# Kernel tuning notes

Hardware: AMD Instinct MI355X
Metric: run time of the kernel (lower is better)

Reference implementation:

```python
import jax, jax.numpy as jnp
import numpy as np

P = 16          # patch_size
C = 3           # in_chans
D = 768         # embed_dim
V = 10240       # position_embedding_size
B, H, W = 16, 512, 512
N = (H // P) * (W // P)  # 1024 patches per image


def setup_inputs() -> dict:
    key = jax.random.key(0)
    k1, k2, k3, k4, k5 = jax.random.split(key, 5)
    pixel_values = jax.random.uniform(k1, (B, C, H, W), dtype=jnp.float32)
    position_ids = jax.random.randint(k2, (B, N, 2), 0, 32)  # (x, y) patch coords < pW/pH
    padding_positions = jax.random.randint(k3, (B, N), 0, 2).astype(jnp.bool_)
    w_proj = jax.random.normal(k4, (D, C * P * P), dtype=jnp.float32) * 0.02  # Linear weight (out, in)
    pos_table = jax.random.normal(k5, (2, V, D), dtype=jnp.float32) * 0.02
    return {
        "pixel_values": pixel_values,
        "w_proj": w_proj,
        "pos_table": pos_table,
        "position_ids": position_ids,
        "padding_positions": padding_positions,
    }


def reference(pixel_values, w_proj, pos_table, position_ids, padding_positions):
    b, c, h, w = pixel_values.shape
    ph, pw = h // P, w // P
    # Extract patches in Gemma4 C-P-P flatten order: (B, N, C*P*P)
    x = pixel_values.reshape(b, c, ph, P, pw, P)
    x = jnp.transpose(x, (0, 2, 4, 1, 3, 5)).reshape(b, ph * pw, c * P * P)
    patches = 2.0 * (x - 0.5)
    hidden = jnp.einsum('bnf,df->bnd', patches, w_proj)
    # Position embeddings: one_hot(ids) @ table summed over the 2 axes
    # == direct gather-add: table[0][x_id] + table[1][y_id]
    ids = jnp.clip(position_ids, 0)
    pos = pos_table[0][ids[..., 0]] + pos_table[1][ids[..., 1]]  # (B, N, D)
    pos = jnp.where(padding_positions[..., None], 0.0, pos)
    return hidden + pos
```

## Files before the change

kernel.cpp:

```cpp
#include <hip/hip_runtime.h>
#include <stdint.h>


typedef __attribute__((ext_vector_type(8))) short bfrag_t;
typedef __attribute__((ext_vector_type(4))) float f4_t;
typedef __attribute__((ext_vector_type(8))) unsigned short u16x8;

#define M_TOT 16384
#define K_TOT 768
#define N_TOT 768
#define V_POS 10240

__device__ __forceinline__ unsigned short f2bf(float f) {
    unsigned int u = __float_as_uint(f);
    u += 0x7fffu + ((u >> 16) & 1u);
    return (unsigned short)(u >> 16);
}

__device__ __forceinline__ void async_ld16(const void* g, void* l) {
    __builtin_amdgcn_global_load_lds(
        (const __attribute__((address_space(1))) void*)g,
        (__attribute__((address_space(3))) void*)l,
        16, 0, 0);
}

__global__ __launch_bounds__(256) void prep_kernel(
    const float* __restrict__ px, const float* __restrict__ wp,
    const void* __restrict__ pad_in,
    unsigned short* __restrict__ A, unsigned short* __restrict__ Wb,
    unsigned char* __restrict__ mask)
{
    int bid = blockIdx.x;
    int tid = threadIdx.x;
    if (bid < 6144) {
        long idx = (long)bid * 256 + tid;
        const float4* s = (const float4*)(px + (idx << 3));
        float4 v0 = s[0];
        float4 v1 = s[1];
        int w8 = (int)(idx & 63);
        int h  = (int)((idx >> 6) & 511);
        int bc = (int)(idx >> 15);
        int c = bc % 3, b = bc / 3;
        int m = b * 1024 + (h >> 4) * 32 + (w8 >> 1);
        int k = c * 256 + (h & 15) * 16 + ((w8 & 1) << 3);
        u16x8 o;
        o[0] = f2bf(2.f * v0.x - 1.f);
        o[1] = f2bf(2.f * v0.y - 1.f);
        o[2] = f2bf(2.f * v0.z - 1.f);
        o[3] = f2bf(2.f * v0.w - 1.f);
        o[4] = f2bf(2.f * v1.x - 1.f);
        o[5] = f2bf(2.f * v1.y - 1.f);
        o[6] = f2bf(2.f * v1.z - 1.f);
        o[7] = f2bf(2.f * v1.w - 1.f);
        *(u16x8*)(A + (long)m * K_TOT + k) = o;
    } else if (bid < 6432) {
        long idx = (long)(bid - 6144) * 256 + tid;
        const float4* s = (const float4*)(wp + (idx << 3));
        float4 v0 = s[0];
        float4 v1 = s[1];
        u16x8 o;
        o[0] = f2bf(v0.x); o[1] = f2bf(v0.y); o[2] = f2bf(v0.z); o[3] = f2bf(v0.w);
        o[4] = f2bf(v1.x); o[5] = f2bf(v1.y); o[6] = f2bf(v1.z); o[7] = f2bf(v1.w);
        *(u16x8*)(Wb + (idx << 3)) = o;
    } else {
        __shared__ int u8mode;
        if (tid == 0) u8mode = 0;
        __syncthreads();
        const unsigned int* pi = (const unsigned int*)pad_in;
        int local = 0;
        for (int i = tid; i < 4096; i += 256)
            if (pi[i] > 1u) local = 1;
        if (local) atomicOr(&u8mode, 1);
        __syncthreads();
        if (u8mode) {
            const unsigned char* p8 = (const unsigned char*)pad_in;
            for (int i = tid; i < M_TOT; i += 256) mask[i] = p8[i];
        } else {
            const int* p32 = (const int*)pad_in;
            for (int i = tid; i < M_TOT; i += 256) mask[i] = (unsigned char)(p32[i] != 0);
        }
    }
}

__global__ __launch_bounds__(256) void gemm_kernel(
    const unsigned short* __restrict__ A, const unsigned short* __restrict__ Bt,
    const int* __restrict__ pos_ids, const unsigned char* __restrict__ mask,
    const float* __restrict__ pos_table, float* __restrict__ out)
{
    __shared__ unsigned short As[128 * 32];
    __shared__ unsigned short Bs[128 * 32];

    int tid  = threadIdx.x;
    int wave = tid >> 6;
    int lane = tid & 63;
    int bm = blockIdx.x / 6, bn = blockIdx.x % 6;
    int m0 = bm * 128, n0 = bn * 128;

    int srow = lane >> 2;
    int scol = (lane & 3) << 3;
    int ch0  = wave * 2;
    const unsigned short* ga0 = A  + (size_t)(m0 + ch0 * 16 +      srow) * K_TOT + scol;
    const unsigned short* ga1 = A  + (size_t)(m0 + ch0 * 16 + 16 + srow) * K_TOT + scol;
    const unsigned short* gb0 = Bt + (size_t)(n0 + ch0 * 16 +      srow) * K_TOT + scol;
    const unsigned short* gb1 = Bt + (size_t)(n0 + ch0 * 16 + 16 + srow) * K_TOT + scol;
    unsigned short* la0 = &As[ch0 * 512];
    unsigned short* la1 = &As[ch0 * 512 + 512];
    unsigned short* lb0 = &Bs[ch0 * 512];
    unsigned short* lb1 = &Bs[ch0 * 512 + 512];

    int row_off = (wave & 1) << 6;
    int col_off = (wave >> 1) << 6;
    int fr = lane & 15;
    int qk = (lane >> 4) << 3;

    f4_t acc[4][4] = {};

    for (int kk = 0; kk < K_TOT / 32; ++kk) {
        int k0 = kk * 32;
        async_ld16(ga0 + k0, la0);
        async_ld16(ga1 + k0, la1);
        async_ld16(gb0 + k0, lb0);
        async_ld16(gb1 + k0, lb1);
        __syncthreads();

        bfrag_t a[4], b[4];
#pragma unroll
        for (int i = 0; i < 4; ++i)
            a[i] = *(const bfrag_t*)&As[(row_off + i * 16 + fr) * 32 + qk];
#pragma unroll
        for (int i = 0; i < 4; ++i)
            b[i] = *(const bfrag_t*)&Bs[(col_off + i * 16 + fr) * 32 + qk];
#pragma unroll
        for (int mi = 0; mi < 4; ++mi)
#pragma unroll
            for (int ni = 0; ni < 4; ++ni)
                acc[mi][ni] = __builtin_amdgcn_mfma_f32_16x16x32_bf16(
                    a[mi], b[ni], acc[mi][ni], 0, 0, 0);
        __syncthreads();
    }

    int quad = lane >> 4;
#pragma unroll
    for (int mi = 0; mi < 4; ++mi) {
#pragma unroll
        for (int reg = 0; reg < 4; ++reg) {
            int r = m0 + row_off + mi * 16 + quad * 4 + reg;
            int xid = pos_ids[2 * r];
            int yid = pos_ids[2 * r + 1];
            xid = xid < 0 ? 0 : xid;
            yid = yid < 0 ? 0 : yid;
            bool p = mask[r] != 0;
            const float* t0 = pos_table + (size_t)xid * N_TOT;
            const float* t1 = pos_table + (size_t)(V_POS + yid) * N_TOT;
            float* orow = out + (size_t)r * N_TOT;
#pragma unroll
            for (int ni = 0; ni < 4; ++ni) {
                int cidx = n0 + col_off + ni * 16 + fr;
                float pos = p ? 0.f : (t0[cidx] + t1[cidx]);
                orow[cidx] = acc[mi][ni][reg] + pos;
            }
        }
    }
}

extern "C" void kernel_launch(void* const* d_in, const int* in_sizes, int n_in,
                              void* d_out, int out_size, void* d_ws, size_t ws_size,
                              hipStream_t stream) {
    const float* px  = (const float*)d_in[0];
    const float* wp  = (const float*)d_in[1];
    const float* pt  = (const float*)d_in[2];
    const int*   pid = (const int*)d_in[3];
    const void*  pad = d_in[4];

    unsigned short* A    = (unsigned short*)d_ws;
    unsigned short* Wb   = A + (size_t)M_TOT * K_TOT;
    unsigned char*  mask = (unsigned char*)(Wb + (size_t)N_TOT * K_TOT);

    prep_kernel<<<6433, 256, 0, stream>>>(px, wp, pad, A, Wb, mask);
    gemm_kernel<<<(M_TOT / 128) * (N_TOT / 128), 256, 0, stream>>>(
        A, Wb, pid, mask, pt, (float*)d_out);
}
```

Measured before the change: 194.1 us.

## Fuse patch extraction into GEMM, stage full-K A tile in LDS, stream B from global

Pixel patch extraction and bf16 conversion now happen inside the GEMM kernel: each block loads one row of 32 patches into LDS with a padded stride, so the bf16 A matrix is no longer written to and re-read from global memory. B fragments are read straight from global/L2 into registers with software double-buffering, and each block loops over all 768 output columns. This removes a large intermediate round trip and one heavy prep pass. The cost is only 512 blocks with a small 32-row M tile, which gives low MFMA reuse per B load and may leave the GPU underoccupied.

```diff
diff --git a/kernel.cpp b/kernel.cpp
--- a/kernel.cpp
+++ b/kernel.cpp
@@ -5,11 +5,13 @@
 typedef __attribute__((ext_vector_type(8))) short bfrag_t;
 typedef __attribute__((ext_vector_type(4))) float f4_t;
 typedef __attribute__((ext_vector_type(8))) unsigned short u16x8;
+typedef __attribute__((ext_vector_type(4))) unsigned short u16x4;
 
 #define M_TOT 16384
 #define K_TOT 768
 #define N_TOT 768
 #define V_POS 10240
+#define A_STRIDE 776
 
 __device__ __forceinline__ unsigned short f2bf(float f) {
     unsigned int u = __float_as_uint(f);
@@ -17,44 +19,13 @@
     return (unsigned short)(u >> 16);
 }
 
-__device__ __forceinline__ void async_ld16(const void* g, void* l) {
-    __builtin_amdgcn_global_load_lds(
-        (const __attribute__((address_space(1))) void*)g,
-        (__attribute__((address_space(3))) void*)l,
-        16, 0, 0);
-}
-
-__global__ __launch_bounds__(256) void prep_kernel(
-    const float* __restrict__ px, const float* __restrict__ wp,
-    const void* __restrict__ pad_in,
-    unsigned short* __restrict__ A, unsigned short* __restrict__ Wb,
-    unsigned char* __restrict__ mask)
+__global__ __launch_bounds__(256) void wprep_kernel(
+    const float* __restrict__ wp, const void* __restrict__ pad_in,
+    unsigned short* __restrict__ Wb, unsigned char* __restrict__ mask)
 {
-    int bid = blockIdx.x;
-    int tid = threadIdx.x;
-    if (bid < 6144) {
+    int bid = blockIdx.x, tid = threadIdx.x;
+    if (bid < 288) {
         long idx = (long)bid * 256 + tid;
-        const float4* s = (const float4*)(px + (idx << 3));
-        float4 v0 = s[0];
-        float4 v1 = s[1];
-        int w8 = (int)(idx & 63);
-        int h  = (int)((idx >> 6) & 511);
-        int bc = (int)(idx >> 15);
-        int c = bc % 3, b = bc / 3;
-        int m = b * 1024 + (h >> 4) * 32 + (w8 >> 1);
-        int k = c * 256 + (h & 15) * 16 + ((w8 & 1) << 3);
-        u16x8 o;
-        o[0] = f2bf(2.f * v0.x - 1.f);
-        o[1] = f2bf(2.f * v0.y - 1.f);
-        o[2] = f2bf(2.f * v0.z - 1.f);
-        o[3] = f2bf(2.f * v0.w - 1.f);
-        o[4] = f2bf(2.f * v1.x - 1.f);
-        o[5] = f2bf(2.f * v1.y - 1.f);
-        o[6] = f2bf(2.f * v1.z - 1.f);
-        o[7] = f2bf(2.f * v1.w - 1.f);
-        *(u16x8*)(A + (long)m * K_TOT + k) = o;
-    } else if (bid < 6432) {
-        long idx = (long)(bid - 6144) * 256 + tid;
         const float4* s = (const float4*)(wp + (idx << 3));
         float4 v0 = s[0];
         float4 v1 = s[1];
@@ -82,82 +53,122 @@
     }
 }
 
-__global__ __launch_bounds__(256) void gemm_kernel(
-    const unsigned short* __restrict__ A, const unsigned short* __restrict__ Bt,
+__global__ __launch_bounds__(256) void fused_kernel(
+    const float* __restrict__ px, const unsigned short* __restrict__ Bt,
     const int* __restrict__ pos_ids, const unsigned char* __restrict__ mask,
     const float* __restrict__ pos_table, float* __restrict__ out)
 {
-    __shared__ unsigned short As[128 * 32];
-    __shared__ unsigned short Bs[128 * 32];
+    __shared__ unsigned short As[32 * A_STRIDE];
 
-    int tid  = threadIdx.x;
-    int wave = tid >> 6;
-    int lane = tid & 63;
-    int bm = blockIdx.x / 6, bn = blockIdx.x % 6;
-    int m0 = bm * 128, n0 = bn * 128;
+    const int tid  = threadIdx.x;
+    const int wave = tid >> 6;
+    const int lane = tid & 63;
+    const int bid  = blockIdx.x;
+    const int b    = bid >> 5;
+    const int ph   = bid & 31;
+    const int m0   = bid << 5;
 
-    int srow = lane >> 2;
-    int scol = (lane & 3) << 3;
-    int ch0  = wave * 2;
-    const unsigned short* ga0 = A  + (size_t)(m0 + ch0 * 16 +      srow) * K_TOT + scol;
-    const unsigned short* ga1 = A  + (size_t)(m0 + ch0 * 16 + 16 + srow) * K_TOT + scol;
-    const unsigned short* gb0 = Bt + (size_t)(n0 + ch0 * 16 +      srow) * K_TOT + scol;
-    const unsigned short* gb1 = Bt + (size_t)(n0 + ch0 * 16 + 16 + srow) * K_TOT + scol;
-    unsigned short* la0 = &As[ch0 * 512];
-    unsigned short* la1 = &As[ch0 * 512 + 512];
-    unsigned short* lb0 = &Bs[ch0 * 512];
-    unsigned short* lb1 = &Bs[ch0 * 512 + 512];
+    const float* pxb = px + ((size_t)b * 3 * 512 + (size_t)ph * 16) * 512;
+#pragma unroll 8
+    for (int it = 0; it < 24; ++it) {
+        int idx = it * 256 + tid;
+        int c   = idx >> 11;
+        int rem = idx & 2047;
+        int hl  = rem >> 7;
+        int w4  = rem & 127;
+        float4 v = *(const float4*)(pxb + (size_t)c * 262144 + hl * 512 + (w4 << 2));
+        int pw  = w4 >> 2;
+        int pxo = (w4 & 3) << 2;
+        int k   = c * 256 + hl * 16 + pxo;
+        u16x4 o;
+        o[0] = f2bf(2.f * v.x - 1.f);
+        o[1] = f2bf(2.f * v.y - 1.f);
+        o[2] = f2bf(2.f * v.z - 1.f);
+        o[3] = f2bf(2.f * v.w - 1.f);
+        *(u16x4*)&As[pw * A_STRIDE + k] = o;
+    }
+    __syncthreads();
 
-    int row_off = (wave & 1) << 6;
-    int col_off = (wave >> 1) << 6;
-    int fr = lane & 15;
-    int qk = (lane >> 4) << 3;
+    const int fr   = lane & 15;
+    const int quad = lane >> 4;
+    const unsigned short* Aq = As + (size_t)fr * A_STRIDE + (quad << 3);
 
-    f4_t acc[4][4] = {};
+    for (int nc = 0; nc < 3; ++nc) {
+        const int colbase = nc * 256 + (wave << 6);
+        const unsigned short* Bw = Bt + (size_t)colbase * K_TOT + (quad << 3);
 
-    for (int kk = 0; kk < K_TOT / 32; ++kk) {
-        int k0 = kk * 32;
-        async_ld16(ga0 + k0, la0);
-        async_ld16(ga1 + k0, la1);
-        async_ld16(gb0 + k0, lb0);
-        async_ld16(gb1 + k0, lb1);
-        __syncthreads();
+        f4_t acc[2][4] = {};
+        bfrag_t a0[2], ac[2], b0[4], b1[4], bc[4];
 
-        bfrag_t a[4], b[4];
 #pragma unroll
-        for (int i = 0; i < 4; ++i)
-            a[i] = *(const bfrag_t*)&As[(row_off + i * 16 + fr) * 32 + qk];
+        for (int ni = 0; ni < 4; ++ni)
+            b0[ni] = *(const bfrag_t*)(Bw + (size_t)(ni * 16 + fr) * K_TOT);
 #pragma unroll
-        for (int i = 0; i < 4; ++i)
-            b[i] = *(const bfrag_t*)&Bs[(col_off + i * 16 + fr) * 32 + qk];
+        for (int ni = 0; ni < 4; ++ni)
+            b1[ni] = *(const bfrag_t*)(Bw + (size_t)(ni * 16 + fr) * K_TOT + 32);
 #pragma unroll
-        for (int mi = 0; mi < 4; ++mi)
+        for (int mi = 0; mi < 2; ++mi)
+            a0[mi] = *(const bfrag_t*)(Aq + (size_t)mi * 16 * A_STRIDE);
+
+        for (int kk = 0; kk < 24; kk += 2) {
+            int kf = (kk + 2 < 24) ? (kk + 2) * 32 : kk * 32;
+#pragma unroll
+            for (int mi = 0; mi < 2; ++mi) ac[mi] = a0[mi];
+#pragma unroll
+            for (int ni = 0; ni < 4; ++ni) bc[ni] = b0[ni];
+#pragma unroll
+            for (int mi = 0; mi < 2; ++mi)
+                a0[mi] = *(const bfrag_t*)(Aq + (size_t)mi * 16 * A_STRIDE + (kk + 1) * 32);
 #pragma unroll
             for (int ni = 0; ni < 4; ++ni)
-                acc[mi][ni] = __builtin_amdgcn_mfma_f32_16x16x32_bf16(
-                    a[mi], b[ni], acc[mi][ni], 0, 0, 0);
-        __syncthreads();
-    }
+                b0[ni] = *(const bfrag_t*)(Bw + (size_t)(ni * 16 + fr) * K_TOT + kf);
+#pragma unroll
+            for (int mi = 0; mi < 2; ++mi)
+#pragma unroll
+                for (int ni = 0; ni < 4; ++ni)
+                    acc[mi][ni] = __builtin_amdgcn_mfma_f32_16x16x32_bf16(
+                        ac[mi], bc[ni], acc[mi][ni], 0, 0, 0);
 
-    int quad = lane >> 4;
+            int kg = (kk + 3 < 24) ? (kk + 3) * 32 : (kk + 1) * 32;
 #pragma unroll
-    for (int mi = 0; mi < 4; ++mi) {
+            for (int mi = 0; mi < 2; ++mi) ac[mi] = a0[mi];
 #pragma unroll
-        for (int reg = 0; reg < 4; ++reg) {
-            int r = m0 + row_off + mi * 16 + quad * 4 + reg;
-            int xid = pos_ids[2 * r];
-            int yid = pos_ids[2 * r + 1];
-            xid = xid < 0 ? 0 : xid;
-            yid = yid < 0 ? 0 : yid;
-            bool p = mask[r] != 0;
-            const float* t0 = pos_table + (size_t)xid * N_TOT;
-            const float* t1 = pos_table + (size_t)(V_POS + yid) * N_TOT;
-            float* orow = out + (size_t)r * N_TOT;
+            for (int ni = 0; ni < 4; ++ni) bc[ni] = b1[ni];
+            if (kk + 2 < 24) {
 #pragma unroll
-            for (int ni = 0; ni < 4; ++ni) {
-                int cidx = n0 + col_off + ni * 16 + fr;
-                float pos = p ? 0.f : (t0[cidx] + t1[cidx]);
-                orow[cidx] = acc[mi][ni][reg] + pos;
+                for (int mi = 0; mi < 2; ++mi)
+                    a0[mi] = *(const bfrag_t*)(Aq + (size_t)mi * 16 * A_STRIDE + (kk + 2) * 32);
+            }
+#pragma unroll
+            for (int ni = 0; ni < 4; ++ni)
+                b1[ni] = *(const bfrag_t*)(Bw + (size_t)(ni * 16 + fr) * K_TOT + kg);
+#pragma unroll
+            for (int mi = 0; mi < 2; ++mi)
+#pragma unroll
+                for (int ni = 0; ni < 4; ++ni)
+                    acc[mi][ni] = __builtin_amdgcn_mfma_f32_16x16x32_bf16(
+                        ac[mi], bc[ni], acc[mi][ni], 0, 0, 0);
+        }
+
+#pragma unroll
+        for (int mi = 0; mi < 2; ++mi) {
+#pragma unroll
+            for (int reg = 0; reg < 4; ++reg) {
+                int gm  = m0 + mi * 16 + (quad << 2) + reg;
+                int xid = pos_ids[2 * gm];
+                int yid = pos_ids[2 * gm + 1];
+                xid = xid < 0 ? 0 : xid;
+                yid = yid < 0 ? 0 : yid;
+                bool p = mask[gm] != 0;
+                const float* t0 = pos_table + (size_t)xid * N_TOT + colbase;
+                const float* t1 = pos_table + (size_t)(V_POS + yid) * N_TOT + colbase;
+                float* orow = out + (size_t)gm * N_TOT + colbase;
+#pragma unroll
+                for (int ni = 0; ni < 4; ++ni) {
+                    int cc = ni * 16 + fr;
+                    float pos = p ? 0.f : (t0[cc] + t1[cc]);
+                    orow[cc] = acc[mi][ni][reg] + pos;
+                }
             }
         }
     }
@@ -172,11 +183,9 @@
     const int*   pid = (const int*)d_in[3];
     const void*  pad = d_in[4];
 
-    unsigned short* A    = (unsigned short*)d_ws;
-    unsigned short* Wb   = A + (size_t)M_TOT * K_TOT;
+    unsigned short* Wb   = (unsigned short*)d_ws;
     unsigned char*  mask = (unsigned char*)(Wb + (size_t)N_TOT * K_TOT);
 
-    prep_kernel<<<6433, 256, 0, stream>>>(px, wp, pad, A, Wb, mask);
-    gemm_kernel<<<(M_TOT / 128) * (N_TOT / 128), 256, 0, stream>>>(
-        A, Wb, pid, mask, pt, (float*)d_out);
+    wprep_kernel<<<289, 256, 0, stream>>>(wp, pad, Wb, mask);
+    fused_kernel<<<512, 256, 0, stream>>>(px, Wb, pid, mask, pt, (float*)d_out);
 }
```

Result: slower. 251.2 us (+29.4%).
